# Performance work log

Hardware: AMD Instinct MI355X
Metric: run time of the kernel (lower is better)

## Reference

```python
import math
import jax, jax.numpy as jnp
import numpy as np

EPS = 1e-7
TOPK = 10
FACTOR_IOU = 6.0
FACTOR_CLS = 0.5


def ciou(b1, b2):
    """Complete IoU. b1, b2 broadcastable [..., 4] boxes (x1,y1,x2,y2)."""
    xi1 = jnp.maximum(b1[..., 0], b2[..., 0])
    yi1 = jnp.maximum(b1[..., 1], b2[..., 1])
    xi2 = jnp.minimum(b1[..., 2], b2[..., 2])
    yi2 = jnp.minimum(b1[..., 3], b2[..., 3])
    inter = jnp.clip(xi2 - xi1, 0) * jnp.clip(yi2 - yi1, 0)
    a1 = (b1[..., 2] - b1[..., 0]) * (b1[..., 3] - b1[..., 1])
    a2 = (b2[..., 2] - b2[..., 0]) * (b2[..., 3] - b2[..., 1])
    union = a1 + a2 - inter
    iou = inter / (union + EPS)
    cx1 = (b1[..., 2] + b1[..., 0]) * 0.5
    cy1 = (b1[..., 3] + b1[..., 1]) * 0.5
    cx2 = (b2[..., 2] + b2[..., 0]) * 0.5
    cy2 = (b2[..., 3] + b2[..., 1]) * 0.5
    cent = (cx1 - cx2) ** 2 + (cy1 - cy2) ** 2
    cw = jnp.maximum(b1[..., 2], b2[..., 2]) - jnp.minimum(b1[..., 0], b2[..., 0])
    ch = jnp.maximum(b1[..., 3], b2[..., 3]) - jnp.minimum(b1[..., 1], b2[..., 1])
    diag = cw ** 2 + ch ** 2 + EPS
    diou = iou - cent / diag
    arctan = (jnp.arctan((b1[..., 2] - b1[..., 0]) / (b1[..., 3] - b1[..., 1] + EPS))
              - jnp.arctan((b2[..., 2] - b2[..., 0]) / (b2[..., 3] - b2[..., 1] + EPS)))
    v = (4.0 / math.pi ** 2) * arctan ** 2
    alpha = jax.lax.stop_gradient(v / (v - iou + 1.0 + EPS))
    return diou - alpha * v


def box_matcher(target, predict_cls, predict_bbox, anchors, class_num):
    """target [B,T,5]; predict_cls [B,A,C] logits; predict_bbox [B,A,4]; anchors [A,2].
    Returns anchor_matched_targets [B,A,C+4], valid_mask [B,A] bool."""
    B, T = target.shape[0], target.shape[1]
    A = anchors.shape[0]
    tcls = jnp.clip(target[..., 0].astype(jnp.int32), 0)        # [B,T]
    tbox = target[..., 1:5]                                       # [B,T,4]

    # grid mask: anchor center inside target box
    ax = anchors[None, None, :, 0]
    ay = anchors[None, None, :, 1]
    grid_mask = ((tbox[:, :, None, 0] < ax) & (ax < tbox[:, :, None, 2])
                 & (tbox[:, :, None, 1] < ay) & (ay < tbox[:, :, None, 3]))  # [B,T,A]

    # pairwise CIoU target x anchor
    iou_mat = jnp.clip(ciou(tbox[:, :, None, :], predict_bbox[:, None, :, :]), 0.0, 1.0)  # [B,T,A]

    # class prob of each target's class at each anchor
    pc = jax.nn.sigmoid(predict_cls)                              # [B,A,C]
    idx_bta = jnp.broadcast_to(tcls[:, :, None], (B, T, A))
    cls_mat = jnp.take_along_axis(pc.transpose(0, 2, 1), idx_bta, axis=1)  # [B,T,A]

    target_matrix = grid_mask * iou_mat ** FACTOR_IOU * cls_mat ** FACTOR_CLS

    # top-k targets per anchor (topk over anchor axis, as in source)
    vals, idx = jax.lax.top_k(target_matrix, TOPK)                # [B,T,K]
    bi = jnp.arange(B)[:, None, None]
    ti = jnp.arange(T)[None, :, None]
    topk_targets = jnp.zeros_like(target_matrix).at[bi, ti, idx].set(vals)
    topk_mask = (topk_targets > 0).astype(jnp.int32)              # [B,T,A]

    # resolve anchors assigned to multiple targets by max IoU
    duplicates = (topk_mask.sum(1, keepdims=True) > 1)            # [B,1,A]
    max_idx = jax.nn.one_hot(jnp.argmax(iou_mat, axis=1), T, dtype=jnp.int32).transpose(0, 2, 1)  # [B,T,A]
    topk_mask = jnp.where(duplicates, max_idx, topk_mask)
    unique_indices = jnp.argmax(topk_mask, axis=1)                # [B,A]
    valid = topk_mask.sum(1)                                      # [B,A]

    align_bbox = jnp.take_along_axis(tbox, jnp.broadcast_to(unique_indices[:, :, None], (B, A, 4)), axis=1)  # [B,A,4]
    align_cls_idx = jnp.take_along_axis(tcls, unique_indices, axis=1)  # [B,A]
    align_cls = jax.nn.one_hot(align_cls_idx, class_num, dtype=target_matrix.dtype)  # [B,A,C]

    iou_m = iou_mat * topk_mask
    tm_m = target_matrix * topk_mask
    max_target = tm_m.max(axis=-1, keepdims=True)                 # [B,T,1]
    max_iou = iou_m.max(axis=-1, keepdims=True)                   # [B,T,1]
    normalize_term = tm_m / (max_target + 1e-9) * max_iou         # [B,T,A]
    normalize_term = jnp.take_along_axis(normalize_term.transpose(0, 2, 1),
                                         unique_indices[:, :, None], axis=2)  # [B,A,1]
    align_cls = align_cls * normalize_term * valid[:, :, None].astype(align_cls.dtype)
    anchor_matched_targets = jnp.concatenate([align_cls, align_bbox], axis=-1)
    return anchor_matched_targets, (valid > 0)


def setup_inputs() -> dict:
    key = jax.random.key(0)
    ks = jax.random.split(key, 6)
    B, T, C = 32, 64, 80
    img = 640.0
    cells = []
    for s in (8, 16, 32):
        n = 640 // s
        xs = (np.arange(n, dtype=np.float32) + 0.5) * s
        gx, gy = np.meshgrid(xs, xs)
        cells.append(np.stack([gx.ravel(), gy.ravel()], axis=1))
    anchors = jnp.asarray(np.concatenate(cells, 0), dtype=jnp.float32)  # [8400,2]
    A = anchors.shape[0]
    cls = jax.random.randint(ks[0], (B, T, 1), 0, C).astype(jnp.float32)
    cxy = jax.random.uniform(ks[1], (B, T, 2)) * img
    wh = jax.random.uniform(ks[2], (B, T, 2)) * 160.0 + 8.0
    tbox = jnp.concatenate([cxy - wh / 2, cxy + wh / 2], axis=-1)
    target = jnp.concatenate([cls, tbox], axis=-1)                # [B,T,5]
    predict_cls = jax.random.normal(ks[3], (B, A, C), dtype=jnp.float32)
    pcxy = anchors[None] + (jax.random.uniform(ks[4], (B, A, 2)) - 0.5) * 32.0
    pwh = jax.random.uniform(ks[5], (B, A, 2)) * 128.0 + 8.0
    predict_bbox = jnp.concatenate([pcxy - pwh / 2, pcxy + pwh / 2], axis=-1)  # [B,A,4]
    return {"target": target, "predict_cls": predict_cls,
            "predict_bbox": predict_bbox, "anchors": anchors}


def reference(target, predict_cls, predict_bbox, anchors):
    C = predict_cls.shape[-1]
    # matcher runs on detached predictions (as in the torch source)
    amt, valid = box_matcher(target,
                             jax.lax.stop_gradient(predict_cls),
                             jax.lax.stop_gradient(predict_bbox),
                             anchors, C)
    targets_cls = amt[..., :C]                                    # [B,A,C]
    targets_bbox = amt[..., C:]                                   # [B,A,4]
    cls_norm = jnp.maximum(targets_cls.sum(), 1.0)
    box_norm = targets_cls.sum(-1)                                # [B,A]

    # BCE-with-logits, sum / cls_norm
    x, t = predict_cls, targets_cls
    bce = jnp.maximum(x, 0) - x * t + jnp.log1p(jnp.exp(-jnp.abs(x)))
    loss_cls = bce.sum() / cls_norm

    # CIoU box loss over valid anchors (elementwise == diag of picked pairwise)
    iou_e = ciou(predict_bbox, targets_bbox)                      # [B,A]
    loss_iou = ((1.0 - iou_e) * box_norm * valid).sum() / cls_norm

    return jnp.stack([loss_iou, loss_cls])
```

## Files before the change

### kernel.cpp

```cpp
#include <hip/hip_runtime.h>
#include <climits>
#include <cmath>


#define NB 32
#define NT 64
#define NA 8400
#define NC 80
#define KTOP 10
#define NE (NT * KTOP)
#define CAP 1024
#define EPSF 1e-7f
#define INV_PI2 0.40528473456935108577f
#define LOG2E_F 1.44269504088896340736f
#define LN2_F   0.69314718055994530942f
#define BCE_BLOCKS 2048

typedef unsigned long long u64;

__device__ __forceinline__ float atan_wh(float x1, float y1, float x2, float y2) {
  return atanf((x2 - x1) / (y2 - y1 + EPSF));
}

__device__ __forceinline__ float ciou_pair(
    float ax1, float ay1, float ax2, float ay2, float atA,
    float bx1, float by1, float bx2, float by2, float atB)
{
  float xi1 = fmaxf(ax1, bx1), yi1 = fmaxf(ay1, by1);
  float xi2 = fminf(ax2, bx2), yi2 = fminf(ay2, by2);
  float inter = fmaxf(xi2 - xi1, 0.f) * fmaxf(yi2 - yi1, 0.f);
  float a1 = (ax2 - ax1) * (ay2 - ay1);
  float a2 = (bx2 - bx1) * (by2 - by1);
  float iou = inter / (a1 + a2 - inter + EPSF);
  float dcx = (ax2 + ax1) * 0.5f - (bx2 + bx1) * 0.5f;
  float dcy = (ay2 + ay1) * 0.5f - (by2 + by1) * 0.5f;
  float cent = dcx * dcx + dcy * dcy;
  float cw = fmaxf(ax2, bx2) - fminf(ax1, bx1);
  float ch = fmaxf(ay2, by2) - fminf(ay1, by1);
  float diag = cw * cw + ch * ch + EPSF;
  float dv = atA - atB;
  float v = INV_PI2 * dv * dv;
  float alpha = v / (v - iou + 1.f + EPSF);
  return iou - cent / diag - alpha * v;
}

__device__ __forceinline__ float softplus_fast(float x) {
  float e = exp2f(-LOG2E_F * fabsf(x));
  float l = __log2f(1.f + e);
  return fmaxf(x, 0.f) + LN2_F * l;
}

__device__ __forceinline__ float sigmoid_fast(float x) {
  return 1.f / (1.f + exp2f(-LOG2E_F * x));
}

__device__ __forceinline__ u64 pack_key(float tm, int a) {
  return ((u64)__float_as_uint(tm) << 32) | (unsigned)(INT_MAX - a);
}

__global__ __launch_bounds__(256) void k_topk(
    const float* __restrict__ target,
    const float* __restrict__ pcls,
    const float* __restrict__ pbox,
    float* __restrict__ top_val, int* __restrict__ top_idx,
    float* __restrict__ top_iou,
    unsigned* __restrict__ mtg, unsigned* __restrict__ mig)
{
  int row = blockIdx.x;
  int tid = threadIdx.x;
  if (tid == 0) { mtg[row] = 0u; mig[row] = 0u; }
  int b = row >> 6;
  const float* tg = target + (size_t)row * 5;
  float tcf = tg[0];
  float x1 = tg[1], y1 = tg[2], x2 = tg[3], y2 = tg[4];
  int tc = (int)tcf; tc = tc < 0 ? 0 : (tc > NC - 1 ? NC - 1 : tc);
  float atan_t = atan_wh(x1, y1, x2, y2);

  __shared__ int s_n;
  __shared__ u64 s_key[CAP];
  __shared__ u64 xw_k[4];
  __shared__ u64 w_key[KTOP];
  if (tid == 0) s_n = 0;
  __syncthreads();

  const float* pb_b = pbox + (size_t)b * NA * 4;
  const float* pc_b = pcls + (size_t)b * NA * NC;

#define LEVEL_LOOP(S, N, BASE)                                              \
  {                                                                         \
    const float s = (float)(S);                                             \
    int ix0 = (int)floorf(x1 / s - 0.5f); if (ix0 < 0) ix0 = 0;             \
    int ix1 = (int)ceilf (x2 / s - 0.5f); if (ix1 > (N)-1) ix1 = (N)-1;     \
    int iy0 = (int)floorf(y1 / s - 0.5f); if (iy0 < 0) iy0 = 0;             \
    int iy1 = (int)ceilf (y2 / s - 0.5f); if (iy1 > (N)-1) iy1 = (N)-1;     \
    int w = ix1 - ix0 + 1; w = w < 0 ? 0 : w;                               \
    int h = iy1 - iy0 + 1; h = h < 0 ? 0 : h;                               \
    int cnt = w * h;                                                        \
    for (int k = tid; k < cnt; k += 256) {                                  \
      int ix = ix0 + k % w;                                                 \
      int iy = iy0 + k / w;                                                 \
      float anx = (ix + 0.5f) * s;                                          \
      float any_ = (iy + 0.5f) * s;                                         \
      if (x1 < anx && anx < x2 && y1 < any_ && any_ < y2) {                 \
        int a = (BASE) + iy * (N) + ix;                                     \
        float4 bb = ((const float4*)pb_b)[a];                               \
        float c = ciou_pair(x1, y1, x2, y2, atan_t, bb.x, bb.y, bb.z, bb.w, \
                            atan_wh(bb.x, bb.y, bb.z, bb.w));               \
        float io = fminf(fmaxf(c, 0.f), 1.f);                               \
        float i2 = io * io;                                                 \
        float i6 = i2 * i2 * i2;                                            \
        float sc = pc_b[(size_t)a * NC + tc];                               \
        float tm = i6 * sqrtf(sigmoid_fast(sc));                            \
        int slot = atomicAdd(&s_n, 1);                                      \
        if (slot < CAP) s_key[slot] = pack_key(tm, a);                      \
      }                                                                     \
    }                                                                       \
  }
  LEVEL_LOOP(8, 80, 0)
  LEVEL_LOOP(16, 40, 6400)
  LEVEL_LOOP(32, 20, 8000)
#undef LEVEL_LOOP
  __syncthreads();
  int n = s_n; if (n > CAP) n = CAP;

  u64 k0 = 0, k1 = 0, k2 = 0, k3 = 0;
  if (tid < n)       k0 = s_key[tid];
  if (tid + 256 < n) k1 = s_key[tid + 256];
  if (tid + 512 < n) k2 = s_key[tid + 512];
  if (tid + 768 < n) k3 = s_key[tid + 768];

  for (int k = 0; k < KTOP; k++) {
    u64 bk = k0;
    if (k1 > bk) bk = k1;
    if (k2 > bk) bk = k2;
    if (k3 > bk) bk = k3;
#pragma unroll
    for (int off = 32; off > 0; off >>= 1) {
      u64 ok = __shfl_xor(bk, off);
      if (ok > bk) bk = ok;
    }
    if ((tid & 63) == 0) xw_k[tid >> 6] = bk;
    __syncthreads();
    u64 fk = xw_k[0];
    if (xw_k[1] > fk) fk = xw_k[1];
    if (xw_k[2] > fk) fk = xw_k[2];
    if (xw_k[3] > fk) fk = xw_k[3];
    if (tid == 0) w_key[k] = fk;
    if (fk != 0) {
      if (k0 == fk) k0 = 0;
      if (k1 == fk) k1 = 0;
      if (k2 == fk) k2 = 0;
      if (k3 == fk) k3 = 0;
    }
    __syncthreads();
  }

  if (tid < KTOP) {
    int k = tid;
    u64 key = w_key[k];
    float v = __uint_as_float((unsigned)(key >> 32));
    int ai = INT_MAX - (int)(key & 0xFFFFFFFFu);
    float io = 0.f;
    if (key != 0 && v > 0.f) {
      float4 bb = ((const float4*)pb_b)[ai];
      float c = ciou_pair(x1, y1, x2, y2, atan_t, bb.x, bb.y, bb.z, bb.w,
                          atan_wh(bb.x, bb.y, bb.z, bb.w));
      io = fminf(fmaxf(c, 0.f), 1.f);
    } else { ai = -1; v = 0.f; }
    size_t o = (size_t)row * KTOP + k;
    top_val[o] = v; top_idx[o] = ai; top_iou[o] = io;
  }
}

__global__ __launch_bounds__(256) void k_resolve(
    const float* __restrict__ target, const float* __restrict__ pcls,
    const float* __restrict__ pbox, const float* __restrict__ anchors,
    const float* __restrict__ top_val, const int* __restrict__ top_idx,
    const float* __restrict__ top_iou,
    float* __restrict__ as_tm, float* __restrict__ as_x,
    float* __restrict__ as_cio, int* __restrict__ as_u,
    unsigned* __restrict__ mtg, unsigned* __restrict__ mig)
{
  int wave = (blockIdx.x * 256 + threadIdx.x) >> 6;
  int lane = threadIdx.x & 63;
  int e0 = wave * 4;
  int b = e0 / NE;

  const float* bv = top_val + (size_t)b * NE;
  const int* bix = top_idx + (size_t)b * NE;

  int ea[4]; float ev[4];
  bool dead[4];
  int cnt[4]; int first[4];
#pragma unroll
  for (int j = 0; j < 4; j++) {
    int el = (e0 - b * NE) + j;
    ev[j] = bv[el]; ea[j] = bix[el];
    dead[j] = (ev[j] <= 0.f);
    cnt[j] = 0; first[j] = NE;
  }

  for (int s = lane; s < NE; s += 64) {
    float v2 = bv[s]; int a2 = bix[s];
    bool live = (v2 > 0.f);
#pragma unroll
    for (int j = 0; j < 4; j++) {
      if (live && a2 == ea[j]) { cnt[j]++; if (s < first[j]) first[j] = s; }
    }
  }
#pragma unroll
  for (int j = 0; j < 4; j++) {
    for (int off = 32; off > 0; off >>= 1) {
      cnt[j] += __shfl_xor(cnt[j], off);
      int of = __shfl_xor(first[j], off);
      first[j] = of < first[j] ? of : first[j];
    }
  }

#pragma unroll
  for (int j = 0; j < 4; j++) {
    int entry = e0 + j;
    int el = (e0 - b * NE) + j;
    if (!dead[j] && first[j] != el) dead[j] = true;
    if (dead[j]) {
      if (lane == 0) { as_tm[entry] = 0.f; as_x[entry] = 0.f;
                       as_cio[entry] = 0.f; as_u[entry] = 0; }
      continue;
    }
    int a = ea[j];
    const float* pb = pbox + ((size_t)b * NA + a) * 4;
    int u; float tm = -1.f, io;
    if (cnt[j] == 1) {
      u = el / KTOP; tm = ev[j]; io = top_iou[entry];
    } else {
      const float* tg = target + (size_t)(b * NT + lane) * 5;
      float tx1 = tg[1], ty1 = tg[2], tx2 = tg[3], ty2 = tg[4];
      float ta = atan_wh(tx1, ty1, tx2, ty2);
      float bx1 = pb[0], by1 = pb[1], bx2 = pb[2], by2 = pb[3];
      float pa = atan_wh(bx1, by1, bx2, by2);
      float c = ciou_pair(tx1, ty1, tx2, ty2, ta, bx1, by1, bx2, by2, pa);
      float cc = fminf(fmaxf(c, 0.f), 1.f);
      float best = cc; int bu = lane;
      for (int off = 32; off > 0; off >>= 1) {
        float ob = __shfl_xor(best, off);
        int ou = __shfl_xor(bu, off);
        if (ob > best || (ob == best && ou < bu)) { best = ob; bu = ou; }
      }
      u = bu; io = best;
    }

    if (lane == 0) {
      const float* tgu = target + (size_t)(b * NT + u) * 5;
      float ux1 = tgu[1], uy1 = tgu[2], ux2 = tgu[3], uy2 = tgu[4];
      int cu = (int)tgu[0]; cu = cu < 0 ? 0 : (cu > NC - 1 ? NC - 1 : cu);
      float x = pcls[((size_t)b * NA + a) * NC + cu];
      if (cnt[j] != 1) {
        float2 an = ((const float2*)anchors)[a];
        float gm = (ux1 < an.x && an.x < ux2 && uy1 < an.y && an.y < uy2)
                       ? 1.f : 0.f;
        float i2 = io * io; float i6 = i2 * i2 * i2;
        float sig = sigmoid_fast(x);
        tm = gm * i6 * sqrtf(sig);
      }
      float bx1 = pb[0], by1 = pb[1], bx2 = pb[2], by2 = pb[3];
      float c = ciou_pair(ux1, uy1, ux2, uy2, atan_wh(ux1, uy1, ux2, uy2),
                          bx1, by1, bx2, by2, atan_wh(bx1, by1, bx2, by2));
      as_tm[entry] = tm; as_x[entry] = x; as_cio[entry] = 1.f - c; as_u[entry] = u;
      atomicMax(&mtg[b * NT + u], __float_as_uint(tm));
      atomicMax(&mig[b * NT + u], __float_as_uint(io));
    }
  }
}

__global__ __launch_bounds__(256) void k_bce_sums(
    const float* __restrict__ pcls,
    const float* __restrict__ as_tm, const float* __restrict__ as_x,
    const float* __restrict__ as_cio, const int* __restrict__ as_u,
    const unsigned* __restrict__ mtg, const unsigned* __restrict__ mig,
    double* __restrict__ bce_part, double* __restrict__ k2_part)
{
  int tid = threadIdx.x;
  __shared__ double red[256];

  if (blockIdx.x < BCE_BLOCKS) {
    const float4* p4 = (const float4*)pcls;
    const int n4 = NB * NA * NC / 4;
    double acc = 0.0;
    for (int i = blockIdx.x * 256 + tid; i < n4; i += BCE_BLOCKS * 256) {
      float4 v = p4[i];
      float p = (softplus_fast(v.x) + softplus_fast(v.y)) +
                (softplus_fast(v.z) + softplus_fast(v.w));
      acc += (double)p;
    }
    red[tid] = acc; __syncthreads();
    for (int off = 128; off > 0; off >>= 1) {
      if (tid < off) red[tid] += red[tid + off];
      __syncthreads();
    }
    if (tid == 0) bce_part[blockIdx.x] = red[0];
    return;
  }

  int b = blockIdx.x - BCE_BLOCKS;
  double s1 = 0.0, s2 = 0.0, s3 = 0.0;
  for (int e = tid; e < NE; e += 256) {
    size_t o = (size_t)b * NE + e;
    float tm = as_tm[o];
    int u = as_u[o];
    float maxt = __uint_as_float(mtg[b * NT + u]);
    float maxi = __uint_as_float(mig[b * NT + u]);
    float nrm = tm / (maxt + 1e-9f) * maxi;
    s1 += (double)nrm;
    s2 += (double)as_x[o] * (double)nrm;
    s3 += (double)(as_cio[o] * nrm);
  }
  red[tid] = s1; __syncthreads();
  for (int off = 128; off > 0; off >>= 1) {
    if (tid < off) red[tid] += red[tid + off];
    __syncthreads();
  }
  if (tid == 0) k2_part[b * 3 + 0] = red[0];
  __syncthreads();
  red[tid] = s2; __syncthreads();
  for (int off = 128; off > 0; off >>= 1) {
    if (tid < off) red[tid] += red[tid + off];
    __syncthreads();
  }
  if (tid == 0) k2_part[b * 3 + 1] = red[0];
  __syncthreads();
  red[tid] = s3; __syncthreads();
  for (int off = 128; off > 0; off >>= 1) {
    if (tid < off) red[tid] += red[tid + off];
    __syncthreads();
  }
  if (tid == 0) k2_part[b * 3 + 2] = red[0];
}

__global__ __launch_bounds__(256) void k_final(const double* __restrict__ bce_part,
                                               const double* __restrict__ k2_part,
                                               float* __restrict__ out) {
  __shared__ double red[256];
  int tid = threadIdx.x;
  double s = 0.0;
  for (int i = tid; i < BCE_BLOCKS; i += 256) s += bce_part[i];
  red[tid] = s; __syncthreads();
  for (int off = 128; off > 0; off >>= 1) {
    if (tid < off) red[tid] += red[tid + off];
    __syncthreads();
  }
  double s4 = red[0]; __syncthreads();

  red[tid] = (tid < NB) ? k2_part[3 * tid + 0] : 0.0; __syncthreads();
  for (int off = 128; off > 0; off >>= 1) {
    if (tid < off) red[tid] += red[tid + off];
    __syncthreads();
  }
  double s1 = red[0]; __syncthreads();

  red[tid] = (tid < NB) ? k2_part[3 * tid + 1] : 0.0; __syncthreads();
  for (int off = 128; off > 0; off >>= 1) {
    if (tid < off) red[tid] += red[tid + off];
    __syncthreads();
  }
  double s2 = red[0]; __syncthreads();

  red[tid] = (tid < NB) ? k2_part[3 * tid + 2] : 0.0; __syncthreads();
  for (int off = 128; off > 0; off >>= 1) {
    if (tid < off) red[tid] += red[tid + off];
    __syncthreads();
  }
  double s3 = red[0];

  if (tid == 0) {
    double cn = fmax(s1, 1.0);
    out[0] = (float)(s3 / cn);
    out[1] = (float)((s4 - s2) / cn);
  }
}

extern "C" void kernel_launch(void* const* d_in, const int* in_sizes, int n_in,
                              void* d_out, int out_size, void* d_ws, size_t ws_size,
                              hipStream_t stream) {
  const float* target  = (const float*)d_in[0];
  const float* pcls    = (const float*)d_in[1];
  const float* pbox    = (const float*)d_in[2];
  const float* anchors = (const float*)d_in[3];
  float* out = (float*)d_out;

  char* ws = (char*)d_ws;
  float*    top_val = (float*)ws;
  int*      top_idx = (int*)(ws + 81920);
  float*    top_iou = (float*)(ws + 163840);
  float*    as_tm   = (float*)(ws + 245760);
  float*    as_x    = (float*)(ws + 327680);
  float*    as_cio  = (float*)(ws + 409600);
  int*      as_u    = (int*)(ws + 491520);
  unsigned* mtg     = (unsigned*)(ws + 573440);
  unsigned* mig     = (unsigned*)(ws + 581632);
  double*   k2_part = (double*)(ws + 589824);
  double*   k3_part = (double*)(ws + 590592);

  k_topk<<<NB * NT, 256, 0, stream>>>(target, pcls, pbox,
                                      top_val, top_idx, top_iou, mtg, mig);
  k_resolve<<<(NB * NE / 4 * 64) / 256, 256, 0, stream>>>(
      target, pcls, pbox, anchors, top_val, top_idx, top_iou,
      as_tm, as_x, as_cio, as_u, mtg, mig);
  k_bce_sums<<<BCE_BLOCKS + NB, 256, 0, stream>>>(
      pcls, as_tm, as_x, as_cio, as_u, mtg, mig, k3_part, k2_part);
  k_final<<<1, 256, 0, stream>>>(k3_part, k2_part, out);
}
```

Measured before the change: 78.02 us.

## Process one target per wavefront in top-k kernel, removing block barriers

The top-k kernel now gives each target row to a single 64-lane wavefront, with four rows per block, in place of a full 256-thread block per row. The shared-memory atomic slot counter is replaced by ballot/popcount compaction. The 10-step top-k selection uses only wave shuffles, so the per-iteration __syncthreads and cross-wave shared reduction disappear. Candidate capacity per row drops to 768 keys. Big target boxes now get less parallelism per row, and any candidates past 768 are silently dropped. A magic-number multiply replaces the integer division.

```diff
diff --git a/kernel.cpp b/kernel.cpp
--- a/kernel.cpp
+++ b/kernel.cpp
@@ -9,7 +9,7 @@
 #define NC 80
 #define KTOP 10
 #define NE (NT * KTOP)
-#define CAP 1024
+#define CAPW 768
 #define EPSF 1e-7f
 #define INV_PI2 0.40528473456935108577f
 #define LOG2E_F 1.44269504088896340736f
@@ -66,9 +66,10 @@
     float* __restrict__ top_iou,
     unsigned* __restrict__ mtg, unsigned* __restrict__ mig)
 {
-  int row = blockIdx.x;
-  int tid = threadIdx.x;
-  if (tid == 0) { mtg[row] = 0u; mig[row] = 0u; }
+  int wv = threadIdx.x >> 6;
+  int lane = threadIdx.x & 63;
+  int row = blockIdx.x * 4 + wv;
+  if (lane == 0) { mtg[row] = 0u; mig[row] = 0u; }
   int b = row >> 6;
   const float* tg = target + (size_t)row * 5;
   float tcf = tg[0];
@@ -76,15 +77,13 @@
   int tc = (int)tcf; tc = tc < 0 ? 0 : (tc > NC - 1 ? NC - 1 : tc);
   float atan_t = atan_wh(x1, y1, x2, y2);
 
-  __shared__ int s_n;
-  __shared__ u64 s_key[CAP];
-  __shared__ u64 xw_k[4];
-  __shared__ u64 w_key[KTOP];
-  if (tid == 0) s_n = 0;
-  __syncthreads();
+  __shared__ u64 s_key[4][CAPW];
+  u64* my = s_key[wv];
 
   const float* pb_b = pbox + (size_t)b * NA * 4;
   const float* pc_b = pcls + (size_t)b * NA * NC;
+
+  int nmine = 0;
 
 #define LEVEL_LOOP(S, N, BASE)                                              \
   {                                                                         \
@@ -96,68 +95,86 @@
     int w = ix1 - ix0 + 1; w = w < 0 ? 0 : w;                               \
     int h = iy1 - iy0 + 1; h = h < 0 ? 0 : h;                               \
     int cnt = w * h;                                                        \
-    for (int k = tid; k < cnt; k += 256) {                                  \
-      int ix = ix0 + k % w;                                                 \
-      int iy = iy0 + k / w;                                                 \
-      float anx = (ix + 0.5f) * s;                                          \
-      float any_ = (iy + 0.5f) * s;                                         \
-      if (x1 < anx && anx < x2 && y1 < any_ && any_ < y2) {                 \
-        int a = (BASE) + iy * (N) + ix;                                     \
-        float4 bb = ((const float4*)pb_b)[a];                               \
-        float c = ciou_pair(x1, y1, x2, y2, atan_t, bb.x, bb.y, bb.z, bb.w, \
-                            atan_wh(bb.x, bb.y, bb.z, bb.w));               \
-        float io = fminf(fmaxf(c, 0.f), 1.f);                               \
-        float i2 = io * io;                                                 \
-        float i6 = i2 * i2 * i2;                                            \
-        float sc = pc_b[(size_t)a * NC + tc];                               \
-        float tm = i6 * sqrtf(sigmoid_fast(sc));                            \
-        int slot = atomicAdd(&s_n, 1);                                      \
-        if (slot < CAP) s_key[slot] = pack_key(tm, a);                      \
+    unsigned magic = w > 0 ? (0xFFFFFFFFu / (unsigned)w) + 1u : 0u;         \
+    for (int k0 = 0; k0 < cnt; k0 += 64) {                                  \
+      int k = k0 + lane;                                                    \
+      bool pred = false; u64 key = 0;                                       \
+      if (k < cnt) {                                                        \
+        int iy = (int)__umulhi((unsigned)k, magic);          \
+        int ix = k - iy * w;                                                \
+        ix += ix0; iy += iy0;                                               \
+        float anx = (ix + 0.5f) * s;                                        \
+        float any_ = (iy + 0.5f) * s;                                       \
+        pred = (x1 < anx && anx < x2 && y1 < any_ && any_ < y2);            \
+        if (pred) {                                                         \
+          int a = (BASE) + iy * (N) + ix;                                   \
+          float4 bb = ((const float4*)pb_b)[a];                             \
+          float c = ciou_pair(x1, y1, x2, y2, atan_t,                       \
+                              bb.x, bb.y, bb.z, bb.w,                       \
+                              atan_wh(bb.x, bb.y, bb.z, bb.w));             \
+          float io = fminf(fmaxf(c, 0.f), 1.f);                             \
+          float i2 = io * io;                                               \
+          float i6 = i2 * i2 * i2;                                          \
+          float sc = pc_b[(size_t)a * NC + tc];                             \
+          float tm = i6 * sqrtf(sigmoid_fast(sc));                         \
+          key = pack_key(tm, a);                                            \
+        }                                                                   \
       }                                                                     \
+      unsigned long long mask = __ballot(pred);                             \
+      if (pred) {                                                           \
+        int slot = nmine + __popcll(mask & ((1ULL << lane) - 1ULL));        \
+        if (slot < CAPW) my[slot] = key;                                    \
+      }                                                                     \
+      nmine += __popcll(mask);                                              \
     }                                                                       \
   }
   LEVEL_LOOP(8, 80, 0)
   LEVEL_LOOP(16, 40, 6400)
   LEVEL_LOOP(32, 20, 8000)
 #undef LEVEL_LOOP
-  __syncthreads();
-  int n = s_n; if (n > CAP) n = CAP;
-
-  u64 k0 = 0, k1 = 0, k2 = 0, k3 = 0;
-  if (tid < n)       k0 = s_key[tid];
-  if (tid + 256 < n) k1 = s_key[tid + 256];
-  if (tid + 512 < n) k2 = s_key[tid + 512];
-  if (tid + 768 < n) k3 = s_key[tid + 768];
-
+  int n = nmine; if (n > CAPW) n = CAPW;
+
+  u64 c0=0,c1=0,c2=0,c3=0,c4=0,c5=0,c6=0,c7=0,c8=0,c9=0,c10=0,c11=0;
+  if (lane < n)            c0  = my[lane];
+  if (lane + 64 < n)       c1  = my[lane + 64];
+  if (lane + 128 < n)      c2  = my[lane + 128];
+  if (lane + 192 < n)      c3  = my[lane + 192];
+  if (lane + 256 < n)      c4  = my[lane + 256];
+  if (lane + 320 < n)      c5  = my[lane + 320];
+  if (lane + 384 < n)      c6  = my[lane + 384];
+  if (lane + 448 < n)      c7  = my[lane + 448];
+  if (lane + 512 < n)      c8  = my[lane + 512];
+  if (lane + 576 < n)      c9  = my[lane + 576];
+  if (lane + 640 < n)      c10 = my[lane + 640];
+  if (lane + 704 < n)      c11 = my[lane + 704];
+
+  u64 winner = 0;
   for (int k = 0; k < KTOP; k++) {
-    u64 bk = k0;
-    if (k1 > bk) bk = k1;
-    if (k2 > bk) bk = k2;
-    if (k3 > bk) bk = k3;
+    u64 bk = c0;
+    if (c1  > bk) bk = c1;   if (c2  > bk) bk = c2;
+    if (c3  > bk) bk = c3;   if (c4  > bk) bk = c4;
+    if (c5  > bk) bk = c5;   if (c6  > bk) bk = c6;
+    if (c7  > bk) bk = c7;   if (c8  > bk) bk = c8;
+    if (c9  > bk) bk = c9;   if (c10 > bk) bk = c10;
+    if (c11 > bk) bk = c11;
 #pragma unroll
     for (int off = 32; off > 0; off >>= 1) {
       u64 ok = __shfl_xor(bk, off);
       if (ok > bk) bk = ok;
     }
-    if ((tid & 63) == 0) xw_k[tid >> 6] = bk;
-    __syncthreads();
-    u64 fk = xw_k[0];
-    if (xw_k[1] > fk) fk = xw_k[1];
-    if (xw_k[2] > fk) fk = xw_k[2];
-    if (xw_k[3] > fk) fk = xw_k[3];
-    if (tid == 0) w_key[k] = fk;
-    if (fk != 0) {
-      if (k0 == fk) k0 = 0;
-      if (k1 == fk) k1 = 0;
-      if (k2 == fk) k2 = 0;
-      if (k3 == fk) k3 = 0;
-    }
-    __syncthreads();
-  }
-
-  if (tid < KTOP) {
-    int k = tid;
-    u64 key = w_key[k];
+    if (lane == k) winner = bk;
+    if (bk != 0) {
+      if (c0  == bk) c0  = 0;  if (c1  == bk) c1  = 0;
+      if (c2  == bk) c2  = 0;  if (c3  == bk) c3  = 0;
+      if (c4  == bk) c4  = 0;  if (c5  == bk) c5  = 0;
+      if (c6  == bk) c6  = 0;  if (c7  == bk) c7  = 0;
+      if (c8  == bk) c8  = 0;  if (c9  == bk) c9  = 0;
+      if (c10 == bk) c10 = 0;  if (c11 == bk) c11 = 0;
+    }
+  }
+
+  if (lane < KTOP) {
+    u64 key = winner;
     float v = __uint_as_float((unsigned)(key >> 32));
     int ai = INT_MAX - (int)(key & 0xFFFFFFFFu);
     float io = 0.f;
@@ -167,7 +184,7 @@
                           atan_wh(bb.x, bb.y, bb.z, bb.w));
       io = fminf(fmaxf(c, 0.f), 1.f);
     } else { ai = -1; v = 0.f; }
-    size_t o = (size_t)row * KTOP + k;
+    size_t o = (size_t)row * KTOP + lane;
     top_val[o] = v; top_idx[o] = ai; top_iou[o] = io;
   }
 }
@@ -400,8 +417,8 @@
   double*   k2_part = (double*)(ws + 589824);
   double*   k3_part = (double*)(ws + 590592);
 
-  k_topk<<<NB * NT, 256, 0, stream>>>(target, pcls, pbox,
-                                      top_val, top_idx, top_iou, mtg, mig);
+  k_topk<<<NB * NT / 4, 256, 0, stream>>>(target, pcls, pbox,
+                                          top_val, top_idx, top_iou, mtg, mig);
   k_resolve<<<(NB * NE / 4 * 64) / 256, 256, 0, stream>>>(
       target, pcls, pbox, anchors, top_val, top_idx, top_iou,
       as_tm, as_x, as_cio, as_u, mtg, mig);
```

Result: faster. 66.18 us, median of 2 (-15.2%).
